# Optimization experiments

Hardware: AMD Instinct MI355X
Metric: run time of the kernel (lower is better)

Reference implementation:

```python
import jax, jax.numpy as jnp
import numpy as np

B, L, D_MODEL = 8, 2048, 768
D_INNER, D_STATE, DT_RANK, K = 1536, 16, 48, 4


def setup_inputs() -> dict:
    key = jax.random.key(0)
    ks = jax.random.split(key, 9)
    s = 0.02
    return {
        "hidden_states": jax.random.normal(ks[0], (B, L, D_MODEL), jnp.float32),
        "W_in": jax.random.normal(ks[1], (D_MODEL, 2 * D_INNER), jnp.float32) * s,
        "conv_w": jax.random.normal(ks[2], (D_INNER, 1, K), jnp.float32) * s,
        "conv_b": jax.random.normal(ks[3], (D_INNER,), jnp.float32) * s,
        "W_x": jax.random.normal(ks[4], (DT_RANK + 2 * D_STATE, D_INNER), jnp.float32) * s,
        "W_dt": jax.random.normal(ks[5], (D_INNER, DT_RANK), jnp.float32) * s,
        "b_dt": jax.random.normal(ks[6], (D_INNER,), jnp.float32) * s,
        "A_log": jax.random.normal(ks[7], (D_INNER, D_STATE), jnp.float32),
        "D_param": jax.random.normal(ks[8], (D_INNER,), jnp.float32),
    }


def _mamba(hidden_states, W_in, conv_w, conv_b, W_x, W_dt, b_dt, A_log, D_param):
    # in_proj then chunk into ssm branch (x) and gating residual (res)
    xz = hidden_states @ W_in                      # (B, L, 2*d_inner)
    x, res = jnp.split(xz, 2, axis=-1)             # each (B, L, d_inner)

    # causal depthwise conv over time, then SiLU
    xc = x.transpose(0, 2, 1)                      # (B, C, L)
    xc = jax.lax.conv_general_dilated(
        xc, conv_w, window_strides=(1,), padding=[(K - 1, 0)],
        feature_group_count=D_INNER, dimension_numbers=("NCH", "OIH", "NCH"))
    x = jax.nn.silu(xc + conv_b[None, :, None]).transpose(0, 2, 1)  # (B, L, d_inner)

    # input-dependent SSM parameters
    x_dbl = x @ W_x.T                              # (B, L, dt_rank + 2*d_state)
    dt = jax.nn.softplus(x_dbl[..., :DT_RANK] @ W_dt.T + b_dt)      # (B, L, d_inner)
    Bm = x_dbl[..., DT_RANK:DT_RANK + D_STATE]     # (B, L, d_state)
    Cm = x_dbl[..., DT_RANK + D_STATE:]            # (B, L, d_state)
    A = -jnp.exp(A_log)                            # (d_inner, d_state)

    def step(h, inp):
        x_t, dt_t, B_t, C_t = inp                  # (B,d_inner),(B,d_inner),(B,d_state),(B,d_state)
        dA = jnp.exp(dt_t[..., None] * A)          # (B, d_inner, d_state)
        dBx = (dt_t * x_t)[..., None] * B_t[:, None, :]
        h = dA * h + dBx
        y = jnp.einsum("bds,bs->bd", h, C_t)
        return h, y

    xs = (x.transpose(1, 0, 2), dt.transpose(1, 0, 2),
          Bm.transpose(1, 0, 2), Cm.transpose(1, 0, 2))
    h0 = jnp.zeros((x.shape[0], D_INNER, D_STATE), x.dtype)
    _, ys = jax.lax.scan(step, h0, xs)             # ys: (L, B, d_inner)
    y = ys.transpose(1, 0, 2) + x * D_param        # skip term
    return y * jax.nn.silu(res)                    # gated output (B, L, d_inner)


def reference(hidden_states, W_in, conv_w, conv_b, W_x, W_dt, b_dt, A_log, D_param):
    return _mamba(hidden_states, W_in, conv_w, conv_b, W_x, W_dt, b_dt, A_log, D_param)
```

## Files before the change

### kernel.cpp

```cpp
#include <hip/hip_runtime.h>
#include <hip/hip_bf16.h>
#include <stdint.h>

#define B_SZ 8
#define L_SZ 2048
#define DM 768
#define DI 1536
#define DS 16
#define DR 48
#define M_SZ (B_SZ * L_SZ)
#define N1 (2 * DI)

#define NC 64
#define TC (L_SZ / NC)
#define CH (B_SZ * DI)
#define KS 2
#define NT2 (DM / 32)
#define L2E 1.44269504088896f

typedef short short8 __attribute__((ext_vector_type(8)));
typedef float f32x4 __attribute__((ext_vector_type(4)));
typedef float f32x2 __attribute__((ext_vector_type(2)));

__device__ __forceinline__ ushort f2b(float f) {
  __hip_bfloat16 h = __float2bfloat16(f);
  return *reinterpret_cast<ushort*>(&h);
}
__device__ __forceinline__ float b2f(ushort u) {
  __hip_bfloat16 h;
  *reinterpret_cast<ushort*>(&h) = u;
  return __bfloat162float(h);
}
__device__ __forceinline__ ushort f2h(float f) {
  _Float16 h = (_Float16)f;
  return *reinterpret_cast<ushort*>(&h);
}
__device__ __forceinline__ float h2f(ushort u) {
  _Float16 h;
  *reinterpret_cast<ushort*>(&h) = u;
  return (float)h;
}

__device__ __forceinline__ void gl16(const ushort* g, ushort* l) {
  __builtin_amdgcn_global_load_lds(
      (const __attribute__((address_space(1))) void*)g,
      (__attribute__((address_space(3))) void*)l, 16, 0, 0);
}


__global__ __launch_bounds__(256) void prep_all(const float4* __restrict__ hs4,
                                                const float* __restrict__ w_in,
                                                const float* __restrict__ wx_f,
                                                const float* __restrict__ wdt_f,
                                                ushort4* __restrict__ A1,
                                                ushort* __restrict__ wt,
                                                ushort* __restrict__ wx_b,
                                                ushort* __restrict__ wdt_p) {
  const int n4 = M_SZ * DM / 4;
  const int nT = 3072 * 96;
  const int nwx = 80 * DI;
  const int nwdt = DI * 64;
  int idx = blockIdx.x * 256 + threadIdx.x;
  if (idx < n4) {
    float4 v = hs4[idx];
    ushort4 o;
    o.x = f2b(v.x); o.y = f2b(v.y); o.z = f2b(v.z); o.w = f2b(v.w);
    A1[idx] = o;
  } else if (idx < n4 + nT) {
    int j = idx - n4;
    int n = j % 3072;
    int kb = (j / 3072) * 8;
    short8 o;
#pragma unroll
    for (int q = 0; q < 8; ++q) o[q] = (short)f2b(w_in[(size_t)(kb + q) * 3072 + n]);
    *(short8*)(wt + (size_t)n * DM + kb) = o;
  } else if (idx < n4 + nT + nwx) {
    int j = idx - n4 - nT;
    wx_b[j] = f2b(wx_f[j]);
  } else if (idx < n4 + nT + nwx + nwdt) {
    int j = idx - n4 - nT - nwx;
    int col = j >> 6, k = j & 63;
    wdt_p[j] = (k < DR) ? f2b(wdt_f[col * DR + k]) : (ushort)0;
  }
}


__global__ __launch_bounds__(512, 1) void gemm_xz(const ushort* __restrict__ A,
                                                  const ushort* __restrict__ Bt,
                                                  ushort* __restrict__ xout,
                                                  ushort* __restrict__ gateout) {
  __shared__ ushort lds[49152];

  const int t = threadIdx.x;
  const int lane = t & 63;
  const int wid = t >> 6;
  const int wm = wid >> 2, wn = wid & 3;
  const int r = lane & 15, hi = lane >> 4;

  const int g = blockIdx.x;
  const int xcd = g & 7;
  const int local = g >> 3;
  const int bx = xcd * 8 + local / 12;
  const int by = local % 12;
  const int bm = bx * 256;
  const int bn = by * 256;

  const ushort* gsrc[4];
  int ldso[4];
#pragma unroll
  for (int i = 0; i < 4; ++i) {
    int c = wid * 4 + i;
    if (c < 16)
      gsrc[i] = A + (size_t)(bm + c * 16 + r) * DM + hi * 8;
    else
      gsrc[i] = Bt + (size_t)(bn + (c - 16) * 16 + r) * DM + hi * 8;
    ldso[i] = c * 512;
  }

  f32x4 acc[8][4];
#pragma unroll
  for (int m = 0; m < 8; ++m)
#pragma unroll
    for (int n = 0; n < 4; ++n) acc[m][n] = f32x4{0.f, 0.f, 0.f, 0.f};

  ushort* b0 = lds;
  ushort* b1 = lds + 16384;
  ushort* b2 = lds + 32768;

#pragma unroll
  for (int i = 0; i < 4; ++i) gl16(gsrc[i], b0 + ldso[i]);
#pragma unroll
  for (int i = 0; i < 4; ++i) gl16(gsrc[i] + 32, b1 + ldso[i]);
  asm volatile("s_waitcnt vmcnt(4)" ::: "memory");
  __builtin_amdgcn_s_barrier();

  for (int kt = 0; kt < NT2; ++kt) {
    const bool stage = (kt + 2 < NT2);
    const int koff = (kt + 2) * 32;

    short8 bfr[4];
#pragma unroll
    for (int n = 0; n < 4; ++n)
      bfr[n] = *(const short8*)&b0[(16 + wn * 4 + n) * 512 + lane * 8];

#pragma unroll
    for (int q = 0; q < 2; ++q) {
      short8 afr[4];
#pragma unroll
      for (int m = 0; m < 4; ++m)
        afr[m] = *(const short8*)&b0[(wm * 8 + q * 4 + m) * 512 + lane * 8];

      if (stage) {
        gl16(gsrc[2 * q] + koff, b2 + ldso[2 * q]);
        gl16(gsrc[2 * q + 1] + koff, b2 + ldso[2 * q + 1]);
      }

      asm volatile("s_barrier" ::: "memory");

      __builtin_amdgcn_s_setprio(1);
#pragma unroll
      for (int m = 0; m < 4; ++m)
#pragma unroll
        for (int n = 0; n < 4; ++n)
          acc[q * 4 + m][n] =
              __builtin_amdgcn_mfma_f32_16x16x32_bf16(afr[m], bfr[n], acc[q * 4 + m][n], 0, 0, 0);
      __builtin_amdgcn_s_setprio(0);

      if (q == 1) {
        if (stage)
          asm volatile("s_waitcnt vmcnt(4)" ::: "memory");
        else
          asm volatile("s_waitcnt vmcnt(0)" ::: "memory");
      }
      asm volatile("s_barrier" ::: "memory");
    }

    ushort* tmp = b0; b0 = b1; b1 = b2; b2 = tmp;
  }

  const bool isx = (bn < DI);
  ushort* outp = isx ? xout : gateout;
  const int cbase = bn - (isx ? 0 : DI) + wn * 64;
#pragma unroll
  for (int mf = 0; mf < 8; ++mf)
#pragma unroll
    for (int nf = 0; nf < 4; ++nf) {
      int col = cbase + nf * 16 + r;
#pragma unroll
      for (int j = 0; j < 4; ++j) {
        int row = bm + wm * 128 + mf * 16 + hi * 4 + j;
        float v = acc[mf][nf][j];
        if (!isx) v = v / (1.f + __expf(-v));
        outp[(size_t)row * DI + col] = f2b(v);
      }
    }
}


__global__ __launch_bounds__(256) void xdbl_conv(const ushort* __restrict__ xp,
                                                 const float* __restrict__ cw,
                                                 const float* __restrict__ cb,
                                                 const ushort* __restrict__ wx,
                                                 ushort* __restrict__ xc,
                                                 float* __restrict__ xdp) {
  __shared__ ushort Af[32 * 544];

  const int tid = threadIdx.x;
  const int row0 = blockIdx.x * 64;
  const int ks = blockIdx.y;

  const int lane = tid & 63, wid = tid >> 6;
  const int r = lane & 15, hi = lane >> 4;
  const int row0w = row0 + wid * 16;

  f32x4 acc[5];
#pragma unroll
  for (int n = 0; n < 5; ++n) acc[n] = f32x4{0.f, 0.f, 0.f, 0.f};

  const int rg = tid >> 5;
  const int c8 = tid & 31;
  const int col_loc = c8 * 8;
  const int chunkc = col_loc >> 5;
  const int hi_w = (col_loc & 31) >> 3;

  for (int sl = 0; sl < 3; ++sl) {
    const int kbeg = ks * 768 + sl * 256;
    if (sl) __syncthreads();

    {
      const int col = kbeg + col_loc;
      float4 cwv[8];
      float cbv[8];
#pragma unroll
      for (int e = 0; e < 8; ++e) {
        cwv[e] = *(const float4*)(cw + (size_t)(col + e) * 4);
        cbv[e] = cb[col + e];
      }
      short8 z8 = {0, 0, 0, 0, 0, 0, 0, 0};
#pragma unroll
      for (int j = 0; j < 8; ++j) {
        int row = row0 + rg * 8 + j;
        int l = row & (L_SZ - 1);
        const ushort* base = xp + (size_t)row * DI + col;
        short8 x0 = *(const short8*)base;
        short8 xm1 = (l >= 1) ? *(const short8*)(base - DI) : z8;
        short8 xm2 = (l >= 2) ? *(const short8*)(base - 2 * DI) : z8;
        short8 xm3 = (l >= 3) ? *(const short8*)(base - 3 * DI) : z8;
        short8 o;
#pragma unroll
        for (int e = 0; e < 8; ++e) {
          float4 w = cwv[e];
          float a = cbv[e] + w.x * b2f((ushort)xm3[e]) + w.y * b2f((ushort)xm2[e]) +
                    w.z * b2f((ushort)xm1[e]) + w.w * b2f((ushort)x0[e]);
          o[e] = (short)f2b(a / (1.f + __expf(-a)));
        }
        *(short8*)(xc + (size_t)row * DI + col) = o;
        int row_loc = rg * 8 + j;
        int chunk = (row_loc >> 4) * 8 + chunkc;
        int lane_t = (hi_w << 4) | (row_loc & 15);
        int slot = lane_t ^ (chunk & 7);
        *(short8*)&Af[chunk * 544 + slot * 8] = o;
      }
    }
    __syncthreads();

#pragma unroll
    for (int k0 = 0; k0 < 8; ++k0) {
      int chunk = wid * 8 + k0;
      short8 a = *(const short8*)&Af[chunk * 544 + ((lane ^ (chunk & 7)) * 8)];
      const int kk = kbeg + k0 * 32;
#pragma unroll
      for (int n = 0; n < 5; ++n) {
        short8 b = *(const short8*)(wx + (size_t)(n * 16 + r) * DI + kk + hi * 8);
        acc[n] = __builtin_amdgcn_mfma_f32_16x16x32_bf16(a, b, acc[n], 0, 0, 0);
      }
    }
  }

  float* op = xdp + (size_t)ks * M_SZ * 80;
#pragma unroll
  for (int n = 0; n < 5; ++n)
#pragma unroll
    for (int j = 0; j < 4; ++j)
      op[(size_t)(row0w + hi * 4 + j) * 80 + n * 16 + r] = acc[n][j];
}

__global__ __launch_bounds__(256) void reduce_xd(const float4* __restrict__ xdp,
                                                 float4* __restrict__ xd) {
  int i = blockIdx.x * 256 + threadIdx.x;
  if (i >= M_SZ * 20) return;
  float4 s = xdp[i];
#pragma unroll
  for (int k = 1; k < KS; ++k) {
    float4 v = xdp[(size_t)k * M_SZ * 20 + i];
    s.x += v.x; s.y += v.y; s.z += v.z; s.w += v.w;
  }
  xd[i] = s;
}


__device__ __forceinline__ short8 pack8f(const float* p) {
  short8 v;
#pragma unroll
  for (int i = 0; i < 8; ++i) v[i] = (short)f2b(p[i]);
  return v;
}

__global__ __launch_bounds__(256) void dt_gemm(const float* __restrict__ xd,
                                               const ushort* __restrict__ wdtp,
                                               const float* __restrict__ bdt,
                                               ushort* __restrict__ dt) {
  int wave = blockIdx.x * 4 + (threadIdx.x >> 6);
  int lane = threadIdx.x & 63;
  int r = lane & 15, hi = lane >> 4;
  int row0 = wave * 16;
  int c0 = blockIdx.y * 64;

  float atmp[8];
  const float* ap = xd + (size_t)(row0 + r) * 80 + hi * 8;
  float4 q0 = *(const float4*)ap, q1 = *(const float4*)(ap + 4);
  atmp[0] = q0.x; atmp[1] = q0.y; atmp[2] = q0.z; atmp[3] = q0.w;
  atmp[4] = q1.x; atmp[5] = q1.y; atmp[6] = q1.z; atmp[7] = q1.w;
  short8 a0 = pack8f(atmp);
  short8 a1 = {0, 0, 0, 0, 0, 0, 0, 0};
  if (hi < 2) {
    const float* ap1 = xd + (size_t)(row0 + r) * 80 + 32 + hi * 8;
    float4 p0 = *(const float4*)ap1, p1 = *(const float4*)(ap1 + 4);
    atmp[0] = p0.x; atmp[1] = p0.y; atmp[2] = p0.z; atmp[3] = p0.w;
    atmp[4] = p1.x; atmp[5] = p1.y; atmp[6] = p1.z; atmp[7] = p1.w;
    a1 = pack8f(atmp);
  }

  f32x4 acc[4];
#pragma unroll
  for (int n = 0; n < 4; ++n) acc[n] = f32x4{0.f, 0.f, 0.f, 0.f};
#pragma unroll
  for (int n = 0; n < 4; ++n) {
    const ushort* wp = wdtp + (size_t)(c0 + n * 16 + r) * 64;
    short8 b0 = *(const short8*)(wp + hi * 8);
    short8 b1 = *(const short8*)(wp + 32 + hi * 8);
    acc[n] = __builtin_amdgcn_mfma_f32_16x16x32_bf16(a0, b0, acc[n], 0, 0, 0);
    acc[n] = __builtin_amdgcn_mfma_f32_16x16x32_bf16(a1, b1, acc[n], 0, 0, 0);
  }
#pragma unroll
  for (int n = 0; n < 4; ++n)
#pragma unroll
    for (int j = 0; j < 4; ++j) {
      int col = c0 + n * 16 + r;
      float z = acc[n][j] + bdt[col];
      float sp = (z > 20.f) ? z : __logf(1.f + __expf(z));
      dt[(size_t)(row0 + hi * 4 + j) * DI + col] = f2h(sp);
    }
}


__global__ __launch_bounds__(256) void scan_pass1(const ushort* __restrict__ dt,
                                                  const ushort* __restrict__ xc,
                                                  const float* __restrict__ xd,
                                                  const float* __restrict__ A_log,
                                                  float* __restrict__ hend,
                                                  float* __restrict__ sumdt) {
  const int d = blockIdx.x * 256 + threadIdx.x;
  const int c = blockIdx.y, b = blockIdx.z;
  const int t0 = c * TC;

  __shared__ float Bs[TC * 16];
  for (int i = threadIdx.x; i < TC * 16; i += 256) {
    int tt = i >> 4, s = i & 15;
    Bs[i] = xd[((size_t)(b * L_SZ + t0 + tt)) * 80 + DR + s];
  }

  f32x2 a2[8];
  const float4* al4 = (const float4*)(A_log + (size_t)d * DS);
#pragma unroll
  for (int q = 0; q < 4; ++q) {
    float4 v = al4[q];
    a2[2 * q] = f32x2{-__expf(v.x) * L2E, -__expf(v.y) * L2E};
    a2[2 * q + 1] = f32x2{-__expf(v.z) * L2E, -__expf(v.w) * L2E};
  }

  __syncthreads();

  f32x2 h2[8];
#pragma unroll
  for (int q = 0; q < 8; ++q) h2[q] = f32x2{0.f, 0.f};
  float sd = 0.f;

  const ushort* dtp = dt + ((size_t)b * L_SZ + t0) * DI + d;
  const ushort* xp = xc + ((size_t)b * L_SZ + t0) * DI + d;

  ushort dt0 = dtp[0], dt1 = dtp[DI];
  ushort xu0 = xp[0], xu1 = xp[DI];
  dtp += 2 * (size_t)DI; xp += 2 * (size_t)DI;
  const f32x4* bp4 = (const f32x4*)Bs;
#pragma unroll 2
  for (int tt = 0; tt < TC; ++tt) {
    ushort dtu = dt0, xu = xu0;
    dt0 = dt1; xu0 = xu1;
    dt1 = *dtp; xu1 = *xp;
    dtp += DI; xp += DI;
    float dtv = h2f(dtu);
    float xv = b2f(xu);
    sd += dtv;
    float dx = dtv * xv;
    f32x2 dts = f32x2{dtv, dtv};
    f32x2 dxs = f32x2{dx, dx};
#pragma unroll
    for (int q4 = 0; q4 < 4; ++q4) {
      f32x4 bq = bp4[q4];
#pragma unroll
      for (int hq = 0; hq < 2; ++hq) {
        int q = q4 * 2 + hq;
        f32x2 bv = f32x2{bq[2 * hq], bq[2 * hq + 1]};
        f32x2 arg, t2;
        asm("v_pk_mul_f32 %0, %1, %2" : "=v"(arg) : "v"(dts), "v"(a2[q]));
        float e0, e1;
        asm("v_exp_f32 %0, %1" : "=v"(e0) : "v"(arg[0]));
        asm("v_exp_f32 %0, %1" : "=v"(e1) : "v"(arg[1]));
        asm("v_pk_mul_f32 %0, %1, %2" : "=v"(t2) : "v"(dxs), "v"(bv));
        h2[q][0] = __builtin_fmaf(e0, h2[q][0], t2[0]);
        h2[q][1] = __builtin_fmaf(e1, h2[q][1], t2[1]);
      }
    }
    bp4 += 4;
  }

  const size_t ch = (size_t)b * DI + d;
  sumdt[ch * NC + c] = sd;
  f32x2* hp = (f32x2*)&hend[((size_t)c * CH + ch) * 16];
#pragma unroll
  for (int q = 0; q < 8; ++q) hp[q] = h2[q];
}


__global__ __launch_bounds__(256) void scan_pass2(const float* __restrict__ A_log,
                                                  const float* __restrict__ sumdt,
                                                  float* __restrict__ hbuf) {
  int idx = blockIdx.x * 256 + threadIdx.x;
  int ch = idx >> 4, s = idx & 15;
  int d = ch % DI;
  float A = -__expf(A_log[d * DS + s]);
  float h = 0.f;
  for (int c = 0; c < NC; ++c) {
    float* p = &hbuf[((size_t)c * CH + ch) * 16 + s];
    float he = *p;
    *p = h;
    float sd = sumdt[(size_t)ch * NC + c];
    h = __expf(A * sd) * h + he;
  }
}

__global__ __launch_bounds__(256) void scan_pass3(const ushort* __restrict__ dt,
                                                  const ushort* __restrict__ xc,
                                                  const float* __restrict__ xd,
                                                  const ushort* __restrict__ gateb,
                                                  const float* __restrict__ A_log,
                                                  const float* __restrict__ Dp,
                                                  const float* __restrict__ hstart,
                                                  float* __restrict__ out) {
  const int d = blockIdx.x * 256 + threadIdx.x;
  const int c = blockIdx.y, b = blockIdx.z;
  const int t0 = c * TC;

  __shared__ float Bs[TC * 16];
  __shared__ float Cs[TC * 16];
  for (int i = threadIdx.x; i < TC * 16; i += 256) {
    int tt = i >> 4, s = i & 15;
    size_t row = ((size_t)(b * L_SZ + t0 + tt)) * 80;
    Bs[i] = xd[row + DR + s];
    Cs[i] = xd[row + DR + DS + s];
  }

  f32x2 a2[8];
  const float4* al4 = (const float4*)(A_log + (size_t)d * DS);
#pragma unroll
  for (int q = 0; q < 4; ++q) {
    float4 v = al4[q];
    a2[2 * q] = f32x2{-__expf(v.x) * L2E, -__expf(v.y) * L2E};
    a2[2 * q + 1] = f32x2{-__expf(v.z) * L2E, -__expf(v.w) * L2E};
  }
  const float Dpv = Dp[d];

  const size_t ch = (size_t)b * DI + d;
  f32x2 h2[8];
  const f32x2* hp = (const f32x2*)&hstart[((size_t)c * CH + ch) * 16];
#pragma unroll
  for (int q = 0; q < 8; ++q) h2[q] = hp[q];

  __syncthreads();

  const ushort* dtp = dt + ((size_t)b * L_SZ + t0) * DI + d;
  const ushort* xp = xc + ((size_t)b * L_SZ + t0) * DI + d;
  const ushort* gp = gateb + ((size_t)b * L_SZ + t0) * DI + d;
  float* op = out + ((size_t)b * L_SZ + t0) * DI + d;

  ushort dt0 = dtp[0], dt1 = dtp[DI];
  ushort xu0 = xp[0], xu1 = xp[DI];
  ushort gu0 = gp[0], gu1 = gp[DI];
  dtp += 2 * (size_t)DI; xp += 2 * (size_t)DI; gp += 2 * (size_t)DI;
  const f32x4* bp4 = (const f32x4*)Bs;
  const f32x4* cp4 = (const f32x4*)Cs;
#pragma unroll 2
  for (int tt = 0; tt < TC; ++tt) {
    ushort dtu = dt0, xu = xu0, gu = gu0;
    dt0 = dt1; xu0 = xu1; gu0 = gu1;
    dt1 = *dtp; xu1 = *xp; gu1 = *gp;
    dtp += DI; xp += DI; gp += DI;
    float dtv = h2f(dtu);
    float xv = b2f(xu);
    float gv = b2f(gu);
    float dx = dtv * xv;
    f32x2 dts = f32x2{dtv, dtv};
    f32x2 dxs = f32x2{dx, dx};
    f32x2 ya = f32x2{0.f, 0.f}, yb = f32x2{0.f, 0.f};
#pragma unroll
    for (int q4 = 0; q4 < 4; ++q4) {
      f32x4 bq = bp4[q4];
      f32x4 cq = cp4[q4];
#pragma unroll
      for (int hq = 0; hq < 2; ++hq) {
        int q = q4 * 2 + hq;
        f32x2 bv = f32x2{bq[2 * hq], bq[2 * hq + 1]};
        f32x2 cv = f32x2{cq[2 * hq], cq[2 * hq + 1]};
        f32x2 arg, t2;
        asm("v_pk_mul_f32 %0, %1, %2" : "=v"(arg) : "v"(dts), "v"(a2[q]));
        float e0, e1;
        asm("v_exp_f32 %0, %1" : "=v"(e0) : "v"(arg[0]));
        asm("v_exp_f32 %0, %1" : "=v"(e1) : "v"(arg[1]));
        asm("v_pk_mul_f32 %0, %1, %2" : "=v"(t2) : "v"(dxs), "v"(bv));
        h2[q][0] = __builtin_fmaf(e0, h2[q][0], t2[0]);
        h2[q][1] = __builtin_fmaf(e1, h2[q][1], t2[1]);
        if (hq)
          asm("v_pk_fma_f32 %0, %1, %2, %0" : "+v"(yb) : "v"(h2[q]), "v"(cv));
        else
          asm("v_pk_fma_f32 %0, %1, %2, %0" : "+v"(ya) : "v"(h2[q]), "v"(cv));
      }
    }
    bp4 += 4; cp4 += 4;
    float y = (ya[0] + ya[1]) + (yb[0] + yb[1]);
    op[0] = (y + xv * Dpv) * gv;
    op += DI;
  }
}


extern "C" void kernel_launch(void* const* d_in, const int* in_sizes, int n_in,
                              void* d_out, int out_size, void* d_ws, size_t ws_size,
                              hipStream_t stream) {
  const float* hs     = (const float*)d_in[0];
  const float* W_in   = (const float*)d_in[1];
  const float* conv_w = (const float*)d_in[2];
  const float* conv_b = (const float*)d_in[3];
  const float* W_x    = (const float*)d_in[4];
  const float* W_dt   = (const float*)d_in[5];
  const float* b_dt   = (const float*)d_in[6];
  const float* A_log  = (const float*)d_in[7];
  const float* D_par  = (const float*)d_in[8];
  float* out = (float*)d_out;
  char* ws = (char*)d_ws;

  size_t o = 0;
  ushort* A1   = (ushort*)(ws + o); o += (size_t)M_SZ * DM * 2;
  ushort* Wt1  = (ushort*)(ws + o); o += (size_t)N1 * DM * 2;
  ushort* xpre = (ushort*)(ws + o); o += (size_t)M_SZ * DI * 2;
  ushort* gate = (ushort*)(ws + o); o += (size_t)M_SZ * DI * 2;
  ushort* xcv  = (ushort*)(ws + o); o += (size_t)M_SZ * DI * 2;
  float*  xdbl = (float*)(ws + o);  o += (size_t)M_SZ * 80 * 4;
  ushort* dtb  = (ushort*)(ws + o); o += (size_t)M_SZ * DI * 2;
  float*  xdp  = (float*)(ws + o);  o += (size_t)KS * M_SZ * 80 * 4;
  ushort* Wxb  = (ushort*)(ws + o); o += (size_t)80 * DI * 2;
  ushort* Wdtp = (ushort*)(ws + o); o += (size_t)DI * 64 * 2;
  if (ws_size < o) return;

  float* hbuf  = (float*)(ws + 0);
  float* sumdt = (float*)(ws + (size_t)NC * CH * 16 * 4);

  const int nprep = M_SZ * DM / 4 + 3072 * 96 + 80 * DI + DI * 64;
  prep_all<<<dim3((nprep + 255) / 256), dim3(256), 0, stream>>>(
      (const float4*)hs, W_in, W_x, W_dt, (ushort4*)A1, Wt1, Wxb, Wdtp);

  gemm_xz<<<dim3((M_SZ / 256) * (N1 / 256)), dim3(512), 0, stream>>>(A1, Wt1, xpre, gate);

  xdbl_conv<<<dim3(M_SZ / 64, KS), dim3(256), 0, stream>>>(xpre, conv_w, conv_b, Wxb,
                                                           xcv, xdp);
  reduce_xd<<<dim3((M_SZ * 20 + 255) / 256), dim3(256), 0, stream>>>((const float4*)xdp, (float4*)xdbl);

  dt_gemm<<<dim3(M_SZ / 64, 24), dim3(256), 0, stream>>>(xdbl, Wdtp, b_dt, dtb);

  scan_pass1<<<dim3(DI / 256, NC, B_SZ), dim3(256), 0, stream>>>(dtb, xcv, xdbl, A_log, hbuf, sumdt);
  scan_pass2<<<dim3(CH * 16 / 256), dim3(256), 0, stream>>>(A_log, sumdt, hbuf);
  scan_pass3<<<dim3(DI / 256, NC, B_SZ), dim3(256), 0, stream>>>(dtb, xcv, xdbl, gate,
                                                                 A_log, D_par, hbuf, out);
}
```

Baseline: 363.1 us.

## Fold split-K partial reduction into consumers and widen dt_gemm column tiles

Removes the reduce_xd kernel. dt_gemm, scan_pass1 and scan_pass3 now each sum the two split-K partial buffers of x_dbl directly when they load them. dt_gemm also loops over six 64-column tiles per block, so the grid drops from 24 to 4 in y and the A operand is loaded and packed once per 384 columns instead of once per 64. This saves one launch and a round-trip of the reduced buffer, but doubles partial-buffer reads in every consumer and reduces dt_gemm parallelism.

```diff
diff --git a/kernel.cpp b/kernel.cpp
--- a/kernel.cpp
+++ b/kernel.cpp
@@ -285,19 +285,6 @@
       op[(size_t)(row0w + hi * 4 + j) * 80 + n * 16 + r] = acc[n][j];
 }
 
-__global__ __launch_bounds__(256) void reduce_xd(const float4* __restrict__ xdp,
-                                                 float4* __restrict__ xd) {
-  int i = blockIdx.x * 256 + threadIdx.x;
-  if (i >= M_SZ * 20) return;
-  float4 s = xdp[i];
-#pragma unroll
-  for (int k = 1; k < KS; ++k) {
-    float4 v = xdp[(size_t)k * M_SZ * 20 + i];
-    s.x += v.x; s.y += v.y; s.z += v.z; s.w += v.w;
-  }
-  xd[i] = s;
-}
-
 
 __device__ __forceinline__ short8 pack8f(const float* p) {
   short8 v;
@@ -306,7 +293,7 @@
   return v;
 }
 
-__global__ __launch_bounds__(256) void dt_gemm(const float* __restrict__ xd,
+__global__ __launch_bounds__(256) void dt_gemm(const float* __restrict__ xdp,
                                                const ushort* __restrict__ wdtp,
                                                const float* __restrict__ bdt,
                                                ushort* __restrict__ dt) {
@@ -314,49 +301,58 @@
   int lane = threadIdx.x & 63;
   int r = lane & 15, hi = lane >> 4;
   int row0 = wave * 16;
-  int c0 = blockIdx.y * 64;
+
+  const float* p0 = xdp + (size_t)(row0 + r) * 80 + hi * 8;
+  const float* p1 = p0 + (size_t)M_SZ * 80;
 
   float atmp[8];
-  const float* ap = xd + (size_t)(row0 + r) * 80 + hi * 8;
-  float4 q0 = *(const float4*)ap, q1 = *(const float4*)(ap + 4);
-  atmp[0] = q0.x; atmp[1] = q0.y; atmp[2] = q0.z; atmp[3] = q0.w;
-  atmp[4] = q1.x; atmp[5] = q1.y; atmp[6] = q1.z; atmp[7] = q1.w;
+  float4 q0 = *(const float4*)p0, q1 = *(const float4*)(p0 + 4);
+  float4 s0 = *(const float4*)p1, s1 = *(const float4*)(p1 + 4);
+  atmp[0] = q0.x + s0.x; atmp[1] = q0.y + s0.y; atmp[2] = q0.z + s0.z; atmp[3] = q0.w + s0.w;
+  atmp[4] = q1.x + s1.x; atmp[5] = q1.y + s1.y; atmp[6] = q1.z + s1.z; atmp[7] = q1.w + s1.w;
   short8 a0 = pack8f(atmp);
   short8 a1 = {0, 0, 0, 0, 0, 0, 0, 0};
   if (hi < 2) {
-    const float* ap1 = xd + (size_t)(row0 + r) * 80 + 32 + hi * 8;
-    float4 p0 = *(const float4*)ap1, p1 = *(const float4*)(ap1 + 4);
-    atmp[0] = p0.x; atmp[1] = p0.y; atmp[2] = p0.z; atmp[3] = p0.w;
-    atmp[4] = p1.x; atmp[5] = p1.y; atmp[6] = p1.z; atmp[7] = p1.w;
+    const float* p0b = p0 + 32 - hi * 8 + hi * 8;
+    const float* q0p = xdp + (size_t)(row0 + r) * 80 + 32 + hi * 8;
+    const float* q1p = q0p + (size_t)M_SZ * 80;
+    float4 u0 = *(const float4*)q0p, u1 = *(const float4*)(q0p + 4);
+    float4 v0 = *(const float4*)q1p, v1 = *(const float4*)(q1p + 4);
+    atmp[0] = u0.x + v0.x; atmp[1] = u0.y + v0.y; atmp[2] = u0.z + v0.z; atmp[3] = u0.w + v0.w;
+    atmp[4] = u1.x + v1.x; atmp[5] = u1.y + v1.y; atmp[6] = u1.z + v1.z; atmp[7] = u1.w + v1.w;
     a1 = pack8f(atmp);
-  }
-
-  f32x4 acc[4];
-#pragma unroll
-  for (int n = 0; n < 4; ++n) acc[n] = f32x4{0.f, 0.f, 0.f, 0.f};
-#pragma unroll
-  for (int n = 0; n < 4; ++n) {
-    const ushort* wp = wdtp + (size_t)(c0 + n * 16 + r) * 64;
-    short8 b0 = *(const short8*)(wp + hi * 8);
-    short8 b1 = *(const short8*)(wp + 32 + hi * 8);
-    acc[n] = __builtin_amdgcn_mfma_f32_16x16x32_bf16(a0, b0, acc[n], 0, 0, 0);
-    acc[n] = __builtin_amdgcn_mfma_f32_16x16x32_bf16(a1, b1, acc[n], 0, 0, 0);
-  }
-#pragma unroll
-  for (int n = 0; n < 4; ++n)
-#pragma unroll
-    for (int j = 0; j < 4; ++j) {
-      int col = c0 + n * 16 + r;
-      float z = acc[n][j] + bdt[col];
-      float sp = (z > 20.f) ? z : __logf(1.f + __expf(z));
-      dt[(size_t)(row0 + hi * 4 + j) * DI + col] = f2h(sp);
-    }
+    (void)p0b;
+  }
+
+  for (int nb = blockIdx.y * 6; nb < blockIdx.y * 6 + 6; ++nb) {
+    int c0 = nb * 64;
+    f32x4 acc[4];
+#pragma unroll
+    for (int n = 0; n < 4; ++n) acc[n] = f32x4{0.f, 0.f, 0.f, 0.f};
+#pragma unroll
+    for (int n = 0; n < 4; ++n) {
+      const ushort* wp = wdtp + (size_t)(c0 + n * 16 + r) * 64;
+      short8 b0 = *(const short8*)(wp + hi * 8);
+      short8 b1 = *(const short8*)(wp + 32 + hi * 8);
+      acc[n] = __builtin_amdgcn_mfma_f32_16x16x32_bf16(a0, b0, acc[n], 0, 0, 0);
+      acc[n] = __builtin_amdgcn_mfma_f32_16x16x32_bf16(a1, b1, acc[n], 0, 0, 0);
+    }
+#pragma unroll
+    for (int n = 0; n < 4; ++n)
+#pragma unroll
+      for (int j = 0; j < 4; ++j) {
+        int col = c0 + n * 16 + r;
+        float z = acc[n][j] + bdt[col];
+        float sp = (z > 20.f) ? z : __logf(1.f + __expf(z));
+        dt[(size_t)(row0 + hi * 4 + j) * DI + col] = f2h(sp);
+      }
+  }
 }
 
 
 __global__ __launch_bounds__(256) void scan_pass1(const ushort* __restrict__ dt,
                                                   const ushort* __restrict__ xc,
-                                                  const float* __restrict__ xd,
+                                                  const float* __restrict__ xdp,
                                                   const float* __restrict__ A_log,
                                                   float* __restrict__ hend,
                                                   float* __restrict__ sumdt) {
@@ -367,7 +363,8 @@
   __shared__ float Bs[TC * 16];
   for (int i = threadIdx.x; i < TC * 16; i += 256) {
     int tt = i >> 4, s = i & 15;
-    Bs[i] = xd[((size_t)(b * L_SZ + t0 + tt)) * 80 + DR + s];
+    size_t row = ((size_t)(b * L_SZ + t0 + tt)) * 80 + DR + s;
+    Bs[i] = xdp[row] + xdp[(size_t)M_SZ * 80 + row];
   }
 
   f32x2 a2[8];
@@ -452,7 +449,7 @@
 
 __global__ __launch_bounds__(256) void scan_pass3(const ushort* __restrict__ dt,
                                                   const ushort* __restrict__ xc,
-                                                  const float* __restrict__ xd,
+                                                  const float* __restrict__ xdp,
                                                   const ushort* __restrict__ gateb,
                                                   const float* __restrict__ A_log,
                                                   const float* __restrict__ Dp,
@@ -467,8 +464,8 @@
   for (int i = threadIdx.x; i < TC * 16; i += 256) {
     int tt = i >> 4, s = i & 15;
     size_t row = ((size_t)(b * L_SZ + t0 + tt)) * 80;
-    Bs[i] = xd[row + DR + s];
-    Cs[i] = xd[row + DR + DS + s];
+    Bs[i] = xdp[row + DR + s] + xdp[(size_t)M_SZ * 80 + row + DR + s];
+    Cs[i] = xdp[row + DR + DS + s] + xdp[(size_t)M_SZ * 80 + row + DR + DS + s];
   }
 
   f32x2 a2[8];
@@ -565,7 +562,6 @@
   ushort* xpre = (ushort*)(ws + o); o += (size_t)M_SZ * DI * 2;
   ushort* gate = (ushort*)(ws + o); o += (size_t)M_SZ * DI * 2;
   ushort* xcv  = (ushort*)(ws + o); o += (size_t)M_SZ * DI * 2;
-  float*  xdbl = (float*)(ws + o);  o += (size_t)M_SZ * 80 * 4;
   ushort* dtb  = (ushort*)(ws + o); o += (size_t)M_SZ * DI * 2;
   float*  xdp  = (float*)(ws + o);  o += (size_t)KS * M_SZ * 80 * 4;
   ushort* Wxb  = (ushort*)(ws + o); o += (size_t)80 * DI * 2;
@@ -583,12 +579,11 @@
 
   xdbl_conv<<<dim3(M_SZ / 64, KS), dim3(256), 0, stream>>>(xpre, conv_w, conv_b, Wxb,
                                                            xcv, xdp);
-  reduce_xd<<<dim3((M_SZ * 20 + 255) / 256), dim3(256), 0, stream>>>((const float4*)xdp, (float4*)xdbl);
-
-  dt_gemm<<<dim3(M_SZ / 64, 24), dim3(256), 0, stream>>>(xdbl, Wdtp, b_dt, dtb);
-
-  scan_pass1<<<dim3(DI / 256, NC, B_SZ), dim3(256), 0, stream>>>(dtb, xcv, xdbl, A_log, hbuf, sumdt);
+
+  dt_gemm<<<dim3(M_SZ / 64, 4), dim3(256), 0, stream>>>(xdp, Wdtp, b_dt, dtb);
+
+  scan_pass1<<<dim3(DI / 256, NC, B_SZ), dim3(256), 0, stream>>>(dtb, xcv, xdp, A_log, hbuf, sumdt);
   scan_pass2<<<dim3(CH * 16 / 256), dim3(256), 0, stream>>>(A_log, sumdt, hbuf);
-  scan_pass3<<<dim3(DI / 256, NC, B_SZ), dim3(256), 0, stream>>>(dtb, xcv, xdbl, gate,
+  scan_pass3<<<dim3(DI / 256, NC, B_SZ), dim3(256), 0, stream>>>(dtb, xcv, xdp, gate,
                                                                  A_log, D_par, hbuf, out);
 }
```

New measurement: 359.7 us. No clear change (-0.9%).
